# Kernel optimization log

Measured on AMD Instinct MI355X. Metric: run time of the kernel, lower is better.

The kernel has to match this reference:

```python
import jax, jax.numpy as jnp
import numpy as np


def setup_inputs() -> dict:
    key = jax.random.key(0)
    kx, kq, kb, kc = jax.random.split(key, 4)
    N, D = 16384, 1024
    x = jax.random.normal(kx, (N, D), dtype=jnp.float32)
    Q = jax.random.normal(kq, (D, D), dtype=jnp.float32)
    b = jax.random.normal(kb, (D,), dtype=jnp.float32)
    c = jax.random.normal(kc, (1,), dtype=jnp.float32)
    return {"x": x, "Q": Q, "b": b, "c": c}


def reference(x, Q, b, c):
    # y_i = x_i^T Q x_i + b^T x_i + c  (same math as diag(x @ Q @ x.T)
    # without materializing the NxN matrix)
    xQ = x @ Q                                # [N, D]
    quad = jnp.sum(xQ * x, axis=-1)           # [N]
    y = quad + x @ b + c                       # [N] (c broadcasts from [1])
    return y[:, None]                          # [N, 1]
```

## Files before the change

kernel.cpp:

```cpp
#include <hip/hip_runtime.h>
#include <hip/hip_bf16.h>


#define DD 1024
#define XR 132

typedef short v8s __attribute__((ext_vector_type(8)));
typedef float v4f __attribute__((ext_vector_type(4)));

__device__ __forceinline__ short f2b(float f) {
    union { __hip_bfloat16 h; short s; } u;
    u.h = __float2bfloat16(f);
    return u.s;
}
__device__ __forceinline__ float b2f(short s) {
    union { unsigned u; float f; } uu;
    uu.u = ((unsigned)(unsigned short)s) << 16;
    return uu.f;
}

#define MFMA16(A, B, C) __builtin_amdgcn_mfma_f32_16x16x32_bf16(A, B, C, 0, 0, 0)

__global__ __launch_bounds__(256, 4)
void cvt_kernel(const float* __restrict__ Q, char* __restrict__ qb)
{
    const int gid = blockIdx.x * 256 + threadIdx.x;
    const int n  = gid >> 7;
    const int k8 = gid & 127;
    const float4 f0 = *(const float4*)(Q + (size_t)n * DD + k8 * 8);
    const float4 f1 = *(const float4*)(Q + (size_t)n * DD + k8 * 8 + 4);
    v8s t;
    t[0]=f2b(f0.x); t[1]=f2b(f0.y); t[2]=f2b(f0.z); t[3]=f2b(f0.w);
    t[4]=f2b(f1.x); t[5]=f2b(f1.y); t[6]=f2b(f1.z); t[7]=f2b(f1.w);
    const int tt = n >> 4, l15 = n & 15;
    const int e = k8 >> 4, rem = k8 & 15, s = rem >> 2, quad = rem & 3;
    char* dst = qb + ((size_t)(tt * 8 + e) << 12) + s * 1024 + (quad * 16 + l15) * 16;
    *(v8s*)dst = t;
}

#define LOADB(B0, B1, B2, B3, T)                                          \
  { const char* p_ = qb + ((size_t)((T) * 8 + e) << 12) + lane * 16;      \
    B0 = *(const v8s*)(p_);                                               \
    B1 = *(const v8s*)(p_ + 1024);                                        \
    B2 = *(const v8s*)(p_ + 2048);                                        \
    B3 = *(const v8s*)(p_ + 3072); }

#define ROUND(B0, B1, B2, B3, T)                                          \
  { const float* xp_ = &xvb[((T) >> 3) & 1][((T) & 7) * 16 + l15];        \
    const float bb_ = (e == 0) ? bvec[(T) * 16 + l15] : 0.f;              \
    v4f c0, c1;                                                           \
    c0 = (v4f){0.f,0.f,0.f,0.f}; c1 = (v4f){0.f,0.f,0.f,0.f};             \
    c0 = MFMA16(a[0][0], B0, c0); c1 = MFMA16(a[1][0], B0, c1);           \
    c0 = MFMA16(a[0][1], B1, c0); c1 = MFMA16(a[1][1], B1, c1);           \
    c0 = MFMA16(a[0][2], B2, c0); c1 = MFMA16(a[1][2], B2, c1);           \
    c0 = MFMA16(a[0][3], B3, c0); c1 = MFMA16(a[1][3], B3, c1);           \
    _Pragma("unroll")                                                     \
    for (int r = 0; r < 4; ++r) {                                         \
      acc[0][r] += (c0[r] + bb_) * xp_[(     quad * 4 + r) * XR];         \
      acc[1][r] += (c1[r] + bb_) * xp_[(16 + quad * 4 + r) * XR];         \
    }                                                                     \
    c0 = (v4f){0.f,0.f,0.f,0.f}; c1 = (v4f){0.f,0.f,0.f,0.f};             \
    c0 = MFMA16(a[2][0], B0, c0); c1 = MFMA16(a[3][0], B0, c1);           \
    c0 = MFMA16(a[2][1], B1, c0); c1 = MFMA16(a[3][1], B1, c1);           \
    c0 = MFMA16(a[2][2], B2, c0); c1 = MFMA16(a[3][2], B2, c1);           \
    c0 = MFMA16(a[2][3], B3, c0); c1 = MFMA16(a[3][3], B3, c1);           \
    _Pragma("unroll")                                                     \
    for (int r = 0; r < 4; ++r) {                                         \
      acc[2][r] += (c0[r] + bb_) * xp_[(32 + quad * 4 + r) * XR];         \
      acc[3][r] += (c1[r] + bb_) * xp_[(48 + quad * 4 + r) * XR];         \
    } }

#define DUMPXV(ph)                                                        \
  { float* bse_ = &xvb[(ph) & 1][0];                                      \
    _Pragma("unroll")                                                     \
    for (int g = 0; g < 4; ++g) {                                         \
      _Pragma("unroll")                                                   \
      for (int s = 0; s < 4; ++s) {                                       \
        float* d_ = bse_ + (g * 16 + l15) * XR + s * 32 + quad * 8;       \
        const v8s fr_ = a[g][s];                                          \
        float4 lo_, hi_;                                                  \
        lo_.x = b2f(fr_[0]); lo_.y = b2f(fr_[1]);                         \
        lo_.z = b2f(fr_[2]); lo_.w = b2f(fr_[3]);                         \
        hi_.x = b2f(fr_[4]); hi_.y = b2f(fr_[5]);                         \
        hi_.z = b2f(fr_[6]); hi_.w = b2f(fr_[7]);                         \
        *(float4*)d_ = lo_; *((float4*)d_ + 1) = hi_;                     \
      } } }

__global__ __launch_bounds__(512, 2)
void quad_kernel(const float* __restrict__ x, const char* __restrict__ qb,
                 const float* __restrict__ bvec, const float* __restrict__ cptr,
                 float* __restrict__ y)
{
    __shared__ __align__(16) float xvb[2][64 * XR];
    __shared__ float yred[8][64];

    const int tid  = threadIdx.x;
    const int lane = tid & 63;
    const int e    = tid >> 6;
    const int quad = lane >> 4;
    const int l15  = lane & 15;

    const int row_base = blockIdx.x * 64;

    v8s bA0, bA1, bA2, bA3, bB0, bB1, bB2, bB3;
    LOADB(bA0, bA1, bA2, bA3, 0);

    v8s a[4][4];
    #pragma unroll
    for (int g = 0; g < 4; ++g) {
        const float* xr = x + (size_t)(row_base + g * 16 + l15) * DD
                        + e * 128 + quad * 8;
        #pragma unroll
        for (int s = 0; s < 4; ++s) {
            const float4 f0 = *(const float4*)(xr + s * 32);
            const float4 f1 = *(const float4*)(xr + s * 32 + 4);
            v8s t;
            t[0]=f2b(f0.x); t[1]=f2b(f0.y); t[2]=f2b(f0.z); t[3]=f2b(f0.w);
            t[4]=f2b(f1.x); t[5]=f2b(f1.y); t[6]=f2b(f1.z); t[7]=f2b(f1.w);
            a[g][s] = t;
            asm volatile("" : "+a"(a[g][s]));
        }
    }

    if (e == 0) DUMPXV(0);
    __syncthreads();

    float acc[4][4];
    #pragma unroll
    for (int g = 0; g < 4; ++g)
        #pragma unroll
        for (int r = 0; r < 4; ++r) acc[g][r] = 0.f;

    for (int t = 0; t < 64; t += 2) {
        if ((t & 7) == 0) {
            if (t) __syncthreads();
            const int ph = (t >> 3) + 1;
            if (ph < 8 && e == ph) DUMPXV(ph);
        }
        LOADB(bB0, bB1, bB2, bB3, t + 1);
        ROUND(bA0, bA1, bA2, bA3, t);
        if (t + 2 < 64) LOADB(bA0, bA1, bA2, bA3, t + 2);
        ROUND(bB0, bB1, bB2, bB3, t + 1);
    }

    #pragma unroll
    for (int g = 0; g < 4; ++g)
        #pragma unroll
        for (int r = 0; r < 4; ++r) {
            float v = acc[g][r];
            v += __shfl_xor(v, 1); v += __shfl_xor(v, 2);
            v += __shfl_xor(v, 4); v += __shfl_xor(v, 8);
            if (l15 == 0)
                yred[e][g * 16 + quad * 4 + r] = v;
        }
    __syncthreads();
    if (tid < 64) {
        float s = yred[0][tid] + yred[1][tid] + yred[2][tid] + yred[3][tid]
                + yred[4][tid] + yred[5][tid] + yred[6][tid] + yred[7][tid];
        y[row_base + tid] = s + cptr[0];
    }
}

extern "C" void kernel_launch(void* const* d_in, const int* in_sizes, int n_in,
                              void* d_out, int out_size, void* d_ws, size_t ws_size,
                              hipStream_t stream)
{
    const float* x = (const float*)d_in[0];
    const float* Q = (const float*)d_in[1];
    const float* b = (const float*)d_in[2];
    const float* c = (const float*)d_in[3];
    float* y = (float*)d_out;
    char* qb = (char*)d_ws;

    cvt_kernel<<<dim3(512), dim3(256), 0, stream>>>(Q, qb);
    quad_kernel<<<dim3(256), dim3(512), 0, stream>>>(x, qb, b, c, y);
}
```

Measured before the change: 184.1 us.

## Transpose shared x staging into half-width phases with vector LDS reads

The shared-memory copy of x is stored transposed (column-major with stride 68), so each lane reads its four row values for an MFMA output tile as one float4 instead of four strided scalar loads. Staging is split into 16 half-width phases of 64 columns to halve the LDS footprint. The round loop is restructured into per-group MFMA chains with incrementing Q pointers, and launch bounds drop to one block per SM. Risks include more barriers (16 instead of 8), scalar transposed LDS writes during staging, and possibly lower occupancy from the launch-bound change.

```diff
diff --git a/kernel.cpp b/kernel.cpp
--- a/kernel.cpp
+++ b/kernel.cpp
@@ -3,7 +3,7 @@
 
 
 #define DD 1024
-#define XR 132
+#define XTR 68
 
 typedef short v8s __attribute__((ext_vector_type(8)));
 typedef float v4f __attribute__((ext_vector_type(4)));
@@ -38,60 +38,39 @@
     *(v8s*)dst = t;
 }
 
-#define LOADB(B0, B1, B2, B3, T)                                          \
-  { const char* p_ = qb + ((size_t)((T) * 8 + e) << 12) + lane * 16;      \
-    B0 = *(const v8s*)(p_);                                               \
-    B1 = *(const v8s*)(p_ + 1024);                                        \
-    B2 = *(const v8s*)(p_ + 2048);                                        \
-    B3 = *(const v8s*)(p_ + 3072); }
+#define LOADB(B0, B1, B2, B3, P)                                          \
+  { B0 = *(const v8s*)(P);                                                \
+    B1 = *(const v8s*)((P) + 1024);                                       \
+    B2 = *(const v8s*)((P) + 2048);                                       \
+    B3 = *(const v8s*)((P) + 3072); }
 
-#define ROUND(B0, B1, B2, B3, T)                                          \
-  { const float* xp_ = &xvb[((T) >> 3) & 1][((T) & 7) * 16 + l15];        \
-    const float bb_ = (e == 0) ? bvec[(T) * 16 + l15] : 0.f;              \
-    v4f c0, c1;                                                           \
-    c0 = (v4f){0.f,0.f,0.f,0.f}; c1 = (v4f){0.f,0.f,0.f,0.f};             \
-    c0 = MFMA16(a[0][0], B0, c0); c1 = MFMA16(a[1][0], B0, c1);           \
-    c0 = MFMA16(a[0][1], B1, c0); c1 = MFMA16(a[1][1], B1, c1);           \
-    c0 = MFMA16(a[0][2], B2, c0); c1 = MFMA16(a[1][2], B2, c1);           \
-    c0 = MFMA16(a[0][3], B3, c0); c1 = MFMA16(a[1][3], B3, c1);           \
+#define DUMP1(BASE, FR, CB, G)                                            \
+  { _Pragma("unroll")                                                     \
+    for (int j = 0; j < 8; ++j)                                           \
+      (BASE)[((CB) + quad * 8 + j) * XTR + (G) * 16 + l15] = b2f((FR)[j]); }
+
+#define ROUND(B0, B1, B2, B3, P, U)                                       \
+  { const float* xq_ = &xvT[(P) & 1][((U) * 16 + l15) * XTR + quad * 4];  \
+    const float bb_ = (e == 0) ? bvec[((P) * 4 + (U)) * 16 + l15] : 0.f;  \
     _Pragma("unroll")                                                     \
-    for (int r = 0; r < 4; ++r) {                                         \
-      acc[0][r] += (c0[r] + bb_) * xp_[(     quad * 4 + r) * XR];         \
-      acc[1][r] += (c1[r] + bb_) * xp_[(16 + quad * 4 + r) * XR];         \
-    }                                                                     \
-    c0 = (v4f){0.f,0.f,0.f,0.f}; c1 = (v4f){0.f,0.f,0.f,0.f};             \
-    c0 = MFMA16(a[2][0], B0, c0); c1 = MFMA16(a[3][0], B0, c1);           \
-    c0 = MFMA16(a[2][1], B1, c0); c1 = MFMA16(a[3][1], B1, c1);           \
-    c0 = MFMA16(a[2][2], B2, c0); c1 = MFMA16(a[3][2], B2, c1);           \
-    c0 = MFMA16(a[2][3], B3, c0); c1 = MFMA16(a[3][3], B3, c1);           \
-    _Pragma("unroll")                                                     \
-    for (int r = 0; r < 4; ++r) {                                         \
-      acc[2][r] += (c0[r] + bb_) * xp_[(32 + quad * 4 + r) * XR];         \
-      acc[3][r] += (c1[r] + bb_) * xp_[(48 + quad * 4 + r) * XR];         \
+    for (int g = 0; g < 4; ++g) {                                         \
+      v4f c_ = (v4f){0.f, 0.f, 0.f, 0.f};                                 \
+      c_ = MFMA16(a[g][0], B0, c_);                                       \
+      c_ = MFMA16(a[g][1], B1, c_);                                       \
+      c_ = MFMA16(a[g][2], B2, c_);                                       \
+      c_ = MFMA16(a[g][3], B3, c_);                                       \
+      const v4f xv_ = *(const v4f*)(xq_ + g * 16);                        \
+      _Pragma("unroll")                                                   \
+      for (int r = 0; r < 4; ++r)                                         \
+        acc[g][r] += (c_[r] + bb_) * xv_[r];                              \
     } }
 
-#define DUMPXV(ph)                                                        \
-  { float* bse_ = &xvb[(ph) & 1][0];                                      \
-    _Pragma("unroll")                                                     \
-    for (int g = 0; g < 4; ++g) {                                         \
-      _Pragma("unroll")                                                   \
-      for (int s = 0; s < 4; ++s) {                                       \
-        float* d_ = bse_ + (g * 16 + l15) * XR + s * 32 + quad * 8;       \
-        const v8s fr_ = a[g][s];                                          \
-        float4 lo_, hi_;                                                  \
-        lo_.x = b2f(fr_[0]); lo_.y = b2f(fr_[1]);                         \
-        lo_.z = b2f(fr_[2]); lo_.w = b2f(fr_[3]);                         \
-        hi_.x = b2f(fr_[4]); hi_.y = b2f(fr_[5]);                         \
-        hi_.z = b2f(fr_[6]); hi_.w = b2f(fr_[7]);                         \
-        *(float4*)d_ = lo_; *((float4*)d_ + 1) = hi_;                     \
-      } } }
-
-__global__ __launch_bounds__(512, 2)
+__global__ __launch_bounds__(512, 1)
 void quad_kernel(const float* __restrict__ x, const char* __restrict__ qb,
                  const float* __restrict__ bvec, const float* __restrict__ cptr,
                  float* __restrict__ y)
 {
-    __shared__ __align__(16) float xvb[2][64 * XR];
+    __shared__ __align__(16) float xvT[2][64 * XTR];
     __shared__ float yred[8][64];
 
     const int tid  = threadIdx.x;
@@ -102,8 +81,10 @@
 
     const int row_base = blockIdx.x * 64;
 
+    const char* qp = qb + ((size_t)e << 12) + lane * 16;
     v8s bA0, bA1, bA2, bA3, bB0, bB1, bB2, bB3;
-    LOADB(bA0, bA1, bA2, bA3, 0);
+    LOADB(bA0, bA1, bA2, bA3, qp);
+    qp += 32768;
 
     v8s a[4][4];
     #pragma unroll
@@ -122,7 +103,14 @@
         }
     }
 
-    if (e == 0) DUMPXV(0);
+    if (e == 0) {
+        float* base = &xvT[0][0];
+        #pragma unroll
+        for (int g = 0; g < 4; ++g) {
+            DUMP1(base, a[g][0],  0, g);
+            DUMP1(base, a[g][1], 32, g);
+        }
+    }
     __syncthreads();
 
     float acc[4][4];
@@ -131,16 +119,35 @@
         #pragma unroll
         for (int r = 0; r < 4; ++r) acc[g][r] = 0.f;
 
-    for (int t = 0; t < 64; t += 2) {
-        if ((t & 7) == 0) {
-            if (t) __syncthreads();
-            const int ph = (t >> 3) + 1;
-            if (ph < 8 && e == ph) DUMPXV(ph);
+    for (int p = 0; p < 16; ++p) {
+        if (p) __syncthreads();
+
+        const int pn = p + 1;
+        if (pn < 16 && e == (pn >> 1)) {
+            float* base = &xvT[pn & 1][0];
+            if (pn & 1) {
+                #pragma unroll
+                for (int g = 0; g < 4; ++g) {
+                    DUMP1(base, a[g][2],  0, g);
+                    DUMP1(base, a[g][3], 32, g);
+                }
+            } else {
+                #pragma unroll
+                for (int g = 0; g < 4; ++g) {
+                    DUMP1(base, a[g][0],  0, g);
+                    DUMP1(base, a[g][1], 32, g);
+                }
+            }
         }
-        LOADB(bB0, bB1, bB2, bB3, t + 1);
-        ROUND(bA0, bA1, bA2, bA3, t);
-        if (t + 2 < 64) LOADB(bA0, bA1, bA2, bA3, t + 2);
-        ROUND(bB0, bB1, bB2, bB3, t + 1);
+
+        LOADB(bB0, bB1, bB2, bB3, qp); qp += 32768;
+        ROUND(bA0, bA1, bA2, bA3, p, 0);
+        LOADB(bA0, bA1, bA2, bA3, qp); qp += 32768;
+        ROUND(bB0, bB1, bB2, bB3, p, 1);
+        LOADB(bB0, bB1, bB2, bB3, qp); qp += 32768;
+        ROUND(bA0, bA1, bA2, bA3, p, 2);
+        if (p < 15) { LOADB(bA0, bA1, bA2, bA3, qp); qp += 32768; }
+        ROUND(bB0, bB1, bB2, bB3, p, 3);
     }
 
     #pragma unroll
```

Result: slower. 275.2 us (+49.5%).
